# Kernel tuning notes

Hardware: AMD Instinct MI355X
Metric: run time of the kernel (lower is better)

Reference implementation:

```python
import jax, jax.numpy as jnp
import numpy as np

S, B, F, H, K = 1024, 128, 202, 100, 19  # seq, batch, in_feat, hidden, num_tags


def setup_inputs() -> dict:
    key = jax.random.key(0)
    ks = jax.random.split(key, 14)
    r = lambda k, sh: jax.random.normal(k, sh, dtype=jnp.float32) * 0.1
    return {
        "x": jax.random.normal(ks[0], (S, B, F), dtype=jnp.float32),
        "W_ih_f": r(ks[1], (H, F)), "W_hh_f": r(ks[2], (H, H)),
        "b_ih_f": r(ks[3], (H,)), "b_hh_f": r(ks[4], (H,)),
        "W_ih_b": r(ks[5], (H, F)), "W_hh_b": r(ks[6], (H, H)),
        "b_ih_b": r(ks[7], (H,)), "b_hh_b": r(ks[8], (H,)),
        "W_out": r(ks[9], (K, 2 * H)), "b_out": r(ks[10], (K,)),
        "start_trans": r(ks[11], (K,)), "end_trans": r(ks[12], (K,)),
        "trans": r(ks[13], (K, K)),
    }


def _rnn_dir(x, W_ih, W_hh, b_ih, b_hh, reverse):
    # Precompute input projection as one big GEMM: (S,B,F) @ (F,H)
    xp = jnp.einsum('sbf,hf->sbh', x, W_ih) + b_ih + b_hh
    h0 = jnp.zeros((x.shape[1], W_hh.shape[0]), x.dtype)

    def step(h, xt):
        h = jnp.tanh(xt + h @ W_hh.T)
        return h, h

    _, hs = jax.lax.scan(step, h0, xp, reverse=reverse)
    return hs  # (S, B, H)


def _viterbi(em, start, end, trans):
    # em: (N, T, K) batch-first emissions (here N=S, T=B due to batch_first quirk)
    em = jnp.swapaxes(em, 0, 1)  # (T, N, K)
    score0 = start + em[0]  # (N, K)

    def step(score, e_t):
        ns = score[:, :, None] + trans[None] + e_t[:, None, :]  # (N, K, K)
        return jnp.max(ns, axis=1), jnp.argmax(ns, axis=1)

    score, hist = jax.lax.scan(step, score0, em[1:])  # hist: (T-1, N, K)
    score = score + end
    last = jnp.argmax(score, axis=1)  # (N,)

    def back(tag, h_t):
        prev = jnp.take_along_axis(h_t, tag[:, None], axis=1)[:, 0]
        return prev, prev

    _, prevs = jax.lax.scan(back, last, hist, reverse=True)  # (T-1, N)
    tags = jnp.concatenate([prevs, last[None]], axis=0)  # (T, N)
    return tags.T  # (N, T)


def reference(x, W_ih_f, W_hh_f, b_ih_f, b_hh_f, W_ih_b, W_hh_b, b_ih_b, b_hh_b,
              W_out, b_out, start_trans, end_trans, trans):
    hf = _rnn_dir(x, W_ih_f, W_hh_f, b_ih_f, b_hh_f, reverse=False)
    hb = _rnn_dir(x, W_ih_b, W_hh_b, b_ih_b, b_hh_b, reverse=True)
    h = jnp.concatenate([hf, hb], axis=-1)  # (S, B, 2H)
    logits = h @ W_out.T + b_out  # (S, B, K)
    em = jax.nn.softmax(logits, axis=2)
    # CRF(batch_first=True) reads dim0 as batch: decode (S,B) tag grid
    tags = _viterbi(em, start_trans, end_trans, trans)  # (S, B) int
    return tags.astype(jnp.float32)
```

## Files before the change

kernel.cpp:

```cpp
#include <hip/hip_runtime.h>
#include <math.h>

#define S_ 1024
#define B_ 128
#define F_ 202
#define H_ 100
#define K_ 19
#define FP_ 208
#define HP_ 128

__global__ __launch_bounds__(256, 1) void rnn_chain_kernel(
    const float* __restrict__ x,
    const float* __restrict__ Wih_f, const float* __restrict__ Whh_f,
    const float* __restrict__ bih_f, const float* __restrict__ bhh_f,
    const float* __restrict__ Wih_b, const float* __restrict__ Whh_b,
    const float* __restrict__ bih_b, const float* __restrict__ bhh_b,
    const float* __restrict__ Wout,
    float* __restrict__ Lbuf)
{
    const int tid = threadIdx.x;
    const int dir = blockIdx.x >> 7;
    const int b   = blockIdx.x & 127;

    const float* Wih = dir ? Wih_b : Wih_f;
    const float* Whh = dir ? Whh_b : Whh_f;
    const float* bih = dir ? bih_b : bih_f;
    const float* bhh = dir ? bhh_b : bhh_f;

    __shared__ __align__(16) float x_buf[2][FP_];
    __shared__ __align__(16) float xp_buf[2][H_];
    __shared__ __align__(16) float h_buf[2][HP_];

    float wih[104];
    float whh[56];
    float wout[16];
    float bias = 0.f;

    const int i   = tid >> 1;
    const int hf_ = tid & 1;

    if (tid < 200) {
        const int f0 = hf_ * 104;
        #pragma unroll
        for (int q = 0; q < 104; ++q) {
            const int f = f0 + q;
            wih[q] = (f < F_) ? Wih[(size_t)i * F_ + f] : 0.f;
        }
        const int j0 = hf_ * 56;
        #pragma unroll
        for (int q = 0; q < 56; ++q) {
            const int j = j0 + q;
            whh[q] = (j < H_) ? Whh[(size_t)i * H_ + j] : 0.f;
        }
        if (hf_ == 0) bias = bih[i] + bhh[i];
    }
    const int lk = tid >> 3;
    const int ls = tid & 7;
    if (tid < 152) {
        #pragma unroll
        for (int q = 0; q < 16; ++q) {
            const int j = ls * 16 + q;
            wout[q] = (j < H_) ? Wout[(size_t)lk * (2 * H_) + dir * H_ + j] : 0.f;
        }
    }

    for (int q = tid; q < FP_; q += 256) { x_buf[0][q] = 0.f; x_buf[1][q] = 0.f; }
    for (int q = tid; q < HP_; q += 256) { h_buf[0][q] = 0.f; h_buf[1][q] = 0.f; }
    __syncthreads();

    {
        const int p0 = dir ? (S_ - 1) : 0;
        const int p1 = dir ? (S_ - 2) : 1;
        const float* r0 = x + ((size_t)p0 * B_ + b) * F_;
        const float* r1 = x + ((size_t)p1 * B_ + b) * F_;
        for (int q = tid; q < F_; q += 256) x_buf[0][q] = r0[q];
        for (int q = tid; q < F_; q += 256) x_buf[1][q] = r1[q];
    }
    __syncthreads();

    auto do_proj = [&](int slot) {
        float a0 = 0.f, a1 = 0.f, a2 = 0.f, a3 = 0.f;
        const float* xb = &x_buf[slot][hf_ * 104];
        #pragma unroll
        for (int q = 0; q < 26; ++q) {
            float4 xv = *(const float4*)(xb + q * 4);
            a0 = fmaf(wih[q * 4 + 0], xv.x, a0);
            a1 = fmaf(wih[q * 4 + 1], xv.y, a1);
            a2 = fmaf(wih[q * 4 + 2], xv.z, a2);
            a3 = fmaf(wih[q * 4 + 3], xv.w, a3);
        }
        float acc = (a0 + a1) + (a2 + a3);
        acc += __shfl_xor(acc, 1);
        if (hf_ == 0) xp_buf[slot][i] = acc + bias;
    };

    auto do_L = [&](int slot, int p) {
        float a0 = 0.f, a1 = 0.f, a2 = 0.f, a3 = 0.f;
        const float* hb = &h_buf[slot][ls * 16];
        #pragma unroll
        for (int q = 0; q < 4; ++q) {
            float4 hv = *(const float4*)(hb + q * 4);
            a0 = fmaf(wout[q * 4 + 0], hv.x, a0);
            a1 = fmaf(wout[q * 4 + 1], hv.y, a1);
            a2 = fmaf(wout[q * 4 + 2], hv.z, a2);
            a3 = fmaf(wout[q * 4 + 3], hv.w, a3);
        }
        float acc = (a0 + a1) + (a2 + a3);
        acc += __shfl_xor(acc, 1);
        acc += __shfl_xor(acc, 2);
        acc += __shfl_xor(acc, 4);
        if (ls == 0) atomicAdd(&Lbuf[((size_t)p * B_ + b) * K_ + lk], acc);
    };

    if (tid < 200) do_proj(0);

    float sreg0 = 0.f, sreg1 = 0.f, sreg2 = 0.f, sreg3 = 0.f;
    const int su = tid - 200;
    if (su >= 0) {
        const int p2 = dir ? (S_ - 3) : 2;
        const float* r = x + ((size_t)p2 * B_ + b) * F_;
        const int f0 = su * 4;
        sreg0 = (f0 + 0 < F_) ? r[f0 + 0] : 0.f;
        sreg1 = (f0 + 1 < F_) ? r[f0 + 1] : 0.f;
        sreg2 = (f0 + 2 < F_) ? r[f0 + 2] : 0.f;
        sreg3 = (f0 + 3 < F_) ? r[f0 + 3] : 0.f;
    }
    __syncthreads();

    for (int t = 0; t < S_; ++t) {
        const int cur = t & 1;
        const int nxt = cur ^ 1;

        if (su >= 0 && t + 2 < S_) {
            const int f0 = su * 4;
            if (f0 + 0 < F_) x_buf[cur][f0 + 0] = sreg0;
            if (f0 + 1 < F_) x_buf[cur][f0 + 1] = sreg1;
            if (f0 + 2 < F_) x_buf[cur][f0 + 2] = sreg2;
            if (f0 + 3 < F_) x_buf[cur][f0 + 3] = sreg3;
        }
        if (su >= 0 && t + 3 < S_) {
            const int p = dir ? (S_ - 4 - t) : (t + 3);
            const float* r = x + ((size_t)p * B_ + b) * F_;
            const int f0 = su * 4;
            sreg0 = (f0 + 0 < F_) ? r[f0 + 0] : 0.f;
            sreg1 = (f0 + 1 < F_) ? r[f0 + 1] : 0.f;
            sreg2 = (f0 + 2 < F_) ? r[f0 + 2] : 0.f;
            sreg3 = (f0 + 3 < F_) ? r[f0 + 3] : 0.f;
        }
        if (tid < 200) {
            float a0 = 0.f, a1 = 0.f, a2 = 0.f, a3 = 0.f;
            const float* hb = &h_buf[cur][hf_ * 56];
            #pragma unroll
            for (int q = 0; q < 14; ++q) {
                float4 hv = *(const float4*)(hb + q * 4);
                a0 = fmaf(whh[q * 4 + 0], hv.x, a0);
                a1 = fmaf(whh[q * 4 + 1], hv.y, a1);
                a2 = fmaf(whh[q * 4 + 2], hv.z, a2);
                a3 = fmaf(whh[q * 4 + 3], hv.w, a3);
            }
            float acc = (a0 + a1) + (a2 + a3);
            acc += __shfl_xor(acc, 1);
            if (hf_ == 0) {
                float v = acc + xp_buf[cur][i];
                h_buf[nxt][i] = tanhf(v);
            }
        }
        if (t >= 1 && tid < 152) {
            const int p = dir ? (S_ - t) : (t - 1);
            do_L(cur, p);
        }
        if (t + 1 < S_ && tid < 200) do_proj(nxt);

        __syncthreads();
    }
    if (tid < 152) {
        const int p = dir ? 0 : (S_ - 1);
        do_L(0, p);
    }
}

__global__ __launch_bounds__(256) void viterbi_kernel(
    const float* __restrict__ Lbuf,
    const float* __restrict__ b_out,
    const float* __restrict__ start_t,
    const float* __restrict__ end_t,
    const float* __restrict__ trans,
    float* __restrict__ out)
{
    const int w    = threadIdx.x >> 6;
    const int lane = threadIdx.x & 63;
    const int n    = blockIdx.x * 4 + w;

    __shared__ float         score_s[4][20];
    __shared__ unsigned char hist_s[4][B_][20];
    __shared__ unsigned char tags_s[4][B_];

    const int kk = (lane < K_) ? lane : 0;
    float tcol[K_];
    #pragma unroll
    for (int j = 0; j < K_; ++j) tcol[j] = trans[j * K_ + kk];
    const float bko = b_out[kk];
    const float stk = start_t[kk];
    const float enk = end_t[kk];

    const float* Lrow = Lbuf + (size_t)n * B_ * K_;

    {
        float lg = -1e30f;
        if (lane < K_) lg = Lrow[kk] + bko;
        float m = lg;
        #pragma unroll
        for (int d = 16; d >= 1; d >>= 1) m = fmaxf(m, __shfl_xor(m, d, 32));
        float pp = (lane < K_) ? expf(lg - m) : 0.f;
        float ssum = pp;
        #pragma unroll
        for (int d = 16; d >= 1; d >>= 1) ssum += __shfl_xor(ssum, d, 32);
        if (lane < K_) score_s[w][lane] = stk + pp / ssum;
    }

    for (int t = 1; t < B_; ++t) {
        float lg = -1e30f;
        if (lane < K_) lg = Lrow[t * K_ + kk] + bko;
        float m = lg;
        #pragma unroll
        for (int d = 16; d >= 1; d >>= 1) m = fmaxf(m, __shfl_xor(m, d, 32));
        float pp = (lane < K_) ? expf(lg - m) : 0.f;
        float ssum = pp;
        #pragma unroll
        for (int d = 16; d >= 1; d >>= 1) ssum += __shfl_xor(ssum, d, 32);
        const float e = pp / ssum;

        float best = -1e30f; int am = 0;
        #pragma unroll
        for (int j = 0; j < K_; ++j) {
            float v = (score_s[w][j] + tcol[j]) + e;
            if (v > best) { best = v; am = j; }
        }
        if (lane < K_) {
            hist_s[w][t][lane] = (unsigned char)am;
            score_s[w][lane]   = best;
        }
    }

    if (lane < K_) score_s[w][lane] += enk;

    if (lane == 0) {
        float bestv = score_s[w][0]; int bi = 0;
        for (int j = 1; j < K_; ++j) {
            float v = score_s[w][j];
            if (v > bestv) { bestv = v; bi = j; }
        }
        int tag = bi;
        tags_s[w][B_ - 1] = (unsigned char)tag;
        for (int t = B_ - 2; t >= 0; --t) {
            tag = hist_s[w][t + 1][tag];
            tags_s[w][t] = (unsigned char)tag;
        }
    }
    out[(size_t)n * B_ + lane]      = (float)tags_s[w][lane];
    out[(size_t)n * B_ + 64 + lane] = (float)tags_s[w][64 + lane];
}

extern "C" void kernel_launch(void* const* d_in, const int* in_sizes, int n_in,
                              void* d_out, int out_size, void* d_ws, size_t ws_size,
                              hipStream_t stream)
{
    const float* x       = (const float*)d_in[0];
    const float* Wih_f   = (const float*)d_in[1];
    const float* Whh_f   = (const float*)d_in[2];
    const float* bih_f   = (const float*)d_in[3];
    const float* bhh_f   = (const float*)d_in[4];
    const float* Wih_b   = (const float*)d_in[5];
    const float* Whh_b   = (const float*)d_in[6];
    const float* bih_b   = (const float*)d_in[7];
    const float* bhh_b   = (const float*)d_in[8];
    const float* Wout    = (const float*)d_in[9];
    const float* b_out   = (const float*)d_in[10];
    const float* start_t = (const float*)d_in[11];
    const float* end_t   = (const float*)d_in[12];
    const float* trans   = (const float*)d_in[13];

    float* Lbuf = (float*)d_ws;
    float* out  = (float*)d_out;

    hipMemsetAsync(Lbuf, 0, (size_t)S_ * B_ * K_ * sizeof(float), stream);

    rnn_chain_kernel<<<dim3(256), dim3(256), 0, stream>>>(
        x, Wih_f, Whh_f, bih_f, bhh_f, Wih_b, Whh_b, bih_b, bhh_b, Wout, Lbuf);

    viterbi_kernel<<<dim3(256), dim3(256), 0, stream>>>(
        Lbuf, b_out, start_t, end_t, trans, out);
}
```

Measured before the change: 1.615 ms.

## Move W_hh to shared memory, keep xp in registers, deepen x prefetch ring

```diff
diff --git a/kernel.cpp b/kernel.cpp
--- a/kernel.cpp
+++ b/kernel.cpp
@@ -6,7 +6,7 @@
 #define F_ 202
 #define H_ 100
 #define K_ 19
-#define FP_ 208
+#define XROW_ 208
 #define HP_ 128
 
 __global__ __launch_bounds__(256, 1) void rnn_chain_kernel(
@@ -27,45 +27,47 @@
     const float* bih = dir ? bih_b : bih_f;
     const float* bhh = dir ? bhh_b : bhh_f;
 
-    __shared__ __align__(16) float x_buf[2][FP_];
-    __shared__ __align__(16) float xp_buf[2][H_];
-    __shared__ __align__(16) float h_buf[2][HP_];
+    __shared__ __align__(16) float  x_buf[4][XROW_];
+    __shared__ __align__(16) float  h_buf[2][HP_];
+    __shared__ __align__(16) float2 whh2_s[56 * H_];
+
+    const int i  = tid >> 1;
+    const int hf = tid & 1;
+    const int lk = tid >> 3;
+    const int ls = tid & 7;
 
     float wih[104];
-    float whh[56];
-    float wout[16];
+    float wlog[16];
     float bias = 0.f;
 
-    const int i   = tid >> 1;
-    const int hf_ = tid & 1;
-
     if (tid < 200) {
-        const int f0 = hf_ * 104;
+        const int f0 = hf * 104;
         #pragma unroll
         for (int q = 0; q < 104; ++q) {
             const int f = f0 + q;
             wih[q] = (f < F_) ? Wih[(size_t)i * F_ + f] : 0.f;
         }
-        const int j0 = hf_ * 56;
-        #pragma unroll
-        for (int q = 0; q < 56; ++q) {
-            const int j = j0 + q;
-            whh[q] = (j < H_) ? Whh[(size_t)i * H_ + j] : 0.f;
-        }
-        if (hf_ == 0) bias = bih[i] + bhh[i];
-    }
-    const int lk = tid >> 3;
-    const int ls = tid & 7;
+        if (hf == 0) bias = bih[i] + bhh[i];
+    }
     if (tid < 152) {
         #pragma unroll
         for (int q = 0; q < 16; ++q) {
             const int j = ls * 16 + q;
-            wout[q] = (j < H_) ? Wout[(size_t)lk * (2 * H_) + dir * H_ + j] : 0.f;
-        }
-    }
-
-    for (int q = tid; q < FP_; q += 256) { x_buf[0][q] = 0.f; x_buf[1][q] = 0.f; }
-    for (int q = tid; q < HP_; q += 256) { h_buf[0][q] = 0.f; h_buf[1][q] = 0.f; }
+            wlog[q] = (j < H_) ? Wout[(size_t)lk * (2 * H_) + dir * H_ + j] : 0.f;
+        }
+    }
+
+    for (int idx = tid; idx < 56 * H_; idx += 256) {
+        const int jj = idx / H_, ii = idx - jj * H_;
+        const int j0 = 2 * jj;
+        float2 v;
+        v.x = (j0     < H_) ? Whh[(size_t)ii * H_ + j0]     : 0.f;
+        v.y = (j0 + 1 < H_) ? Whh[(size_t)ii * H_ + j0 + 1] : 0.f;
+        whh2_s[idx] = v;
+    }
+
+    for (int q = tid; q < 4 * XROW_; q += 256) (&x_buf[0][0])[q] = 0.f;
+    for (int q = tid; q < 2 * HP_; q += 256) (&h_buf[0][0])[q] = 0.f;
     __syncthreads();
 
     {
@@ -73,109 +75,152 @@
         const int p1 = dir ? (S_ - 2) : 1;
         const float* r0 = x + ((size_t)p0 * B_ + b) * F_;
         const float* r1 = x + ((size_t)p1 * B_ + b) * F_;
-        for (int q = tid; q < F_; q += 256) x_buf[0][q] = r0[q];
-        for (int q = tid; q < F_; q += 256) x_buf[1][q] = r1[q];
+        if (tid < F_) { x_buf[0][tid] = r0[tid]; x_buf[1][tid] = r1[tid]; }
     }
     __syncthreads();
 
-    auto do_proj = [&](int slot) {
+    const int sl = tid - 192;
+    const int e0 = sl;
+    const int e1 = sl + 64;
+    float2 sA0 = {0.f, 0.f}, sA1 = {0.f, 0.f};
+    float2 sB0 = {0.f, 0.f}, sB1 = {0.f, 0.f};
+    if (tid >= 192) {
+        const int pa = dir ? (S_ - 3) : 2;
+        const int pb = dir ? (S_ - 4) : 3;
+        const float* ra = x + ((size_t)pa * B_ + b) * F_;
+        const float* rb = x + ((size_t)pb * B_ + b) * F_;
+        sA0 = *(const float2*)(ra + e0 * 2);
+        if (e1 < 101) sA1 = *(const float2*)(ra + e1 * 2);
+        sB0 = *(const float2*)(rb + e0 * 2);
+        if (e1 < 101) sB1 = *(const float2*)(rb + e1 * 2);
+    }
+
+    float xp_cur = 0.f, xp_nxt = 0.f;
+    if (tid < 200) {
         float a0 = 0.f, a1 = 0.f, a2 = 0.f, a3 = 0.f;
-        const float* xb = &x_buf[slot][hf_ * 104];
+        const float* xb = &x_buf[0][hf * 104];
         #pragma unroll
         for (int q = 0; q < 26; ++q) {
-            float4 xv = *(const float4*)(xb + q * 4);
-            a0 = fmaf(wih[q * 4 + 0], xv.x, a0);
-            a1 = fmaf(wih[q * 4 + 1], xv.y, a1);
-            a2 = fmaf(wih[q * 4 + 2], xv.z, a2);
-            a3 = fmaf(wih[q * 4 + 3], xv.w, a3);
+            const float4 xv = *(const float4*)(xb + q * 4);
+            a0 = fmaf(wih[q*4+0], xv.x, a0);
+            a1 = fmaf(wih[q*4+1], xv.y, a1);
+            a2 = fmaf(wih[q*4+2], xv.z, a2);
+            a3 = fmaf(wih[q*4+3], xv.w, a3);
         }
         float acc = (a0 + a1) + (a2 + a3);
         acc += __shfl_xor(acc, 1);
-        if (hf_ == 0) xp_buf[slot][i] = acc + bias;
+        xp_cur = acc + bias;
+    }
+    __syncthreads();
+
+    auto STEP = [&](int t, float2& r0, float2& r1) {
+        const int rh = t & 1;
+        const int wh = rh ^ 1;
+        const int rx = (t + 1) & 3;
+
+        if (tid >= 192) {
+            if (t + 2 < S_) {
+                const int ws = (t + 2) & 3;
+                *(float2*)&x_buf[ws][e0 * 2] = r0;
+                if (e1 < 101) *(float2*)&x_buf[ws][e1 * 2] = r1;
+            }
+            if (t + 4 < S_) {
+                const int p = dir ? (S_ - 5 - t) : (t + 4);
+                const float* rr = x + ((size_t)p * B_ + b) * F_;
+                r0 = *(const float2*)(rr + e0 * 2);
+                if (e1 < 101) r1 = *(const float2*)(rr + e1 * 2);
+            }
+        }
+
+        float rsum = 0.f;
+        if (tid < 200) {
+            float a0 = 0.f, a1 = 0.f, a2 = 0.f, a3 = 0.f;
+            const float*  hb = &h_buf[rh][hf * 56];
+            const float2* wp = &whh2_s[(size_t)(hf * 28) * H_ + i];
+            #pragma unroll
+            for (int q = 0; q < 14; ++q) {
+                const float4 hv  = *(const float4*)(hb + q * 4);
+                const float2 w01 = wp[(2 * q)     * H_];
+                const float2 w23 = wp[(2 * q + 1) * H_];
+                a0 = fmaf(w01.x, hv.x, a0);
+                a1 = fmaf(w01.y, hv.y, a1);
+                a2 = fmaf(w23.x, hv.z, a2);
+                a3 = fmaf(w23.y, hv.w, a3);
+            }
+            float acc = (a0 + a1) + (a2 + a3);
+            acc += __shfl_xor(acc, 1);
+            rsum = acc + xp_cur;
+        }
+
+        if (t >= 1 && tid < 152) {
+            float a0 = 0.f, a1 = 0.f, a2 = 0.f, a3 = 0.f;
+            const float* hb2 = &h_buf[rh][ls * 16];
+            #pragma unroll
+            for (int q = 0; q < 4; ++q) {
+                const float4 hv = *(const float4*)(hb2 + q * 4);
+                a0 = fmaf(wlog[q*4+0], hv.x, a0);
+                a1 = fmaf(wlog[q*4+1], hv.y, a1);
+                a2 = fmaf(wlog[q*4+2], hv.z, a2);
+                a3 = fmaf(wlog[q*4+3], hv.w, a3);
+            }
+            float acc = (a0 + a1) + (a2 + a3);
+            acc += __shfl_xor(acc, 1);
+            acc += __shfl_xor(acc, 2);
+            acc += __shfl_xor(acc, 4);
+            if (ls == 0) {
+                const int pl = dir ? (S_ - t) : (t - 1);
+                atomicAdd(&Lbuf[((size_t)pl * B_ + b) * K_ + lk], acc);
+            }
+        }
+
+        if (tid < 200 && hf == 0) h_buf[wh][i] = tanhf(rsum);
+
+        if (t + 1 < S_ && tid < 200) {
+            float a0 = 0.f, a1 = 0.f, a2 = 0.f, a3 = 0.f;
+            const float* xb = &x_buf[rx][hf * 104];
+            #pragma unroll
+            for (int q = 0; q < 26; ++q) {
+                const float4 xv = *(const float4*)(xb + q * 4);
+                a0 = fmaf(wih[q*4+0], xv.x, a0);
+                a1 = fmaf(wih[q*4+1], xv.y, a1);
+                a2 = fmaf(wih[q*4+2], xv.z, a2);
+                a3 = fmaf(wih[q*4+3], xv.w, a3);
+            }
+            float acc = (a0 + a1) + (a2 + a3);
+            acc += __shfl_xor(acc, 1);
+            xp_nxt = acc + bias;
+        }
+        xp_cur = xp_nxt;
+
+        __asm__ volatile("s_waitcnt lgkmcnt(0)" ::: "memory");
+        __builtin_amdgcn_s_barrier();
+        __asm__ volatile("" ::: "memory");
     };
 
-    auto do_L = [&](int slot, int p) {
+    for (int t2 = 0; t2 < S_; t2 += 2) {
+        STEP(t2,     sA0, sA1);
+        STEP(t2 + 1, sB0, sB1);
+    }
+
+    if (tid < 152) {
         float a0 = 0.f, a1 = 0.f, a2 = 0.f, a3 = 0.f;
-        const float* hb = &h_buf[slot][ls * 16];
+        const float* hb2 = &h_buf[0][ls * 16];
         #pragma unroll
         for (int q = 0; q < 4; ++q) {
-            float4 hv = *(const float4*)(hb + q * 4);
-            a0 = fmaf(wout[q * 4 + 0], hv.x, a0);
-            a1 = fmaf(wout[q * 4 + 1], hv.y, a1);
-            a2 = fmaf(wout[q * 4 + 2], hv.z, a2);
-            a3 = fmaf(wout[q * 4 + 3], hv.w, a3);
+            const float4 hv = *(const float4*)(hb2 + q * 4);
+            a0 = fmaf(wlog[q*4+0], hv.x, a0);
+            a1 = fmaf(wlog[q*4+1], hv.y, a1);
+            a2 = fmaf(wlog[q*4+2], hv.z, a2);
+            a3 = fmaf(wlog[q*4+3], hv.w, a3);
         }
         float acc = (a0 + a1) + (a2 + a3);
         acc += __shfl_xor(acc, 1);
         acc += __shfl_xor(acc, 2);
         acc += __shfl_xor(acc, 4);
-        if (ls == 0) atomicAdd(&Lbuf[((size_t)p * B_ + b) * K_ + lk], acc);
-    };
-
-    if (tid < 200) do_proj(0);
-
-    float sreg0 = 0.f, sreg1 = 0.f, sreg2 = 0.f, sreg3 = 0.f;
-    const int su = tid - 200;
-    if (su >= 0) {
-        const int p2 = dir ? (S_ - 3) : 2;
-        const float* r = x + ((size_t)p2 * B_ + b) * F_;
-        const int f0 = su * 4;
-        sreg0 = (f0 + 0 < F_) ? r[f0 + 0] : 0.f;
-        sreg1 = (f0 + 1 < F_) ? r[f0 + 1] : 0.f;
-        sreg2 = (f0 + 2 < F_) ? r[f0 + 2] : 0.f;
-        sreg3 = (f0 + 3 < F_) ? r[f0 + 3] : 0.f;
-    }
-    __syncthreads();
-
-    for (int t = 0; t < S_; ++t) {
-        const int cur = t & 1;
-        const int nxt = cur ^ 1;
-
-        if (su >= 0 && t + 2 < S_) {
-            const int f0 = su * 4;
-            if (f0 + 0 < F_) x_buf[cur][f0 + 0] = sreg0;
-            if (f0 + 1 < F_) x_buf[cur][f0 + 1] = sreg1;
-            if (f0 + 2 < F_) x_buf[cur][f0 + 2] = sreg2;
-            if (f0 + 3 < F_) x_buf[cur][f0 + 3] = sreg3;
-        }
-        if (su >= 0 && t + 3 < S_) {
-            const int p = dir ? (S_ - 4 - t) : (t + 3);
-            const float* r = x + ((size_t)p * B_ + b) * F_;
-            const int f0 = su * 4;
-            sreg0 = (f0 + 0 < F_) ? r[f0 + 0] : 0.f;
-            sreg1 = (f0 + 1 < F_) ? r[f0 + 1] : 0.f;
-            sreg2 = (f0 + 2 < F_) ? r[f0 + 2] : 0.f;
-            sreg3 = (f0 + 3 < F_) ? r[f0 + 3] : 0.f;
-        }
-        if (tid < 200) {
-            float a0 = 0.f, a1 = 0.f, a2 = 0.f, a3 = 0.f;
-            const float* hb = &h_buf[cur][hf_ * 56];
-            #pragma unroll
-            for (int q = 0; q < 14; ++q) {
-                float4 hv = *(const float4*)(hb + q * 4);
-                a0 = fmaf(whh[q * 4 + 0], hv.x, a0);
-                a1 = fmaf(whh[q * 4 + 1], hv.y, a1);
-                a2 = fmaf(whh[q * 4 + 2], hv.z, a2);
-                a3 = fmaf(whh[q * 4 + 3], hv.w, a3);
-            }
-            float acc = (a0 + a1) + (a2 + a3);
-            acc += __shfl_xor(acc, 1);
-            if (hf_ == 0) {
-                float v = acc + xp_buf[cur][i];
-                h_buf[nxt][i] = tanhf(v);
-            }
-        }
-        if (t >= 1 && tid < 152) {
-            const int p = dir ? (S_ - t) : (t - 1);
-            do_L(cur, p);
-        }
-        if (t + 1 < S_ && tid < 200) do_proj(nxt);
-
-        __syncthreads();
-    }
-    if (tid < 152) {
-        const int p = dir ? 0 : (S_ - 1);
-        do_L(0, p);
+        if (ls == 0) {
+            const int pl = dir ? 0 : (S_ - 1);
+            atomicAdd(&Lbuf[((size_t)pl * B_ + b) * K_ + lk], acc);
+        }
     }
 }
 
@@ -233,7 +278,7 @@
         float best = -1e30f; int am = 0;
         #pragma unroll
         for (int j = 0; j < K_; ++j) {
-            float v = (score_s[w][j] + tcol[j]) + e;
+            const float v = (score_s[w][j] + tcol[j]) + e;
             if (v > best) { best = v; am = j; }
         }
         if (lane < K_) {
@@ -247,7 +292,7 @@
     if (lane == 0) {
         float bestv = score_s[w][0]; int bi = 0;
         for (int j = 1; j < K_; ++j) {
-            float v = score_s[w][j];
+            const float v = score_s[w][j];
             if (v > bestv) { bestv = v; bi = j; }
         }
         int tag = bi;
```

After: 1.676 ms. 1.04x slower.
